# Optimization experiments

Measured on AMD Instinct MI355X. Metric: run time of the kernel, lower is better.

## Reference

```python
import jax, jax.numpy as jnp
import numpy as np

B, T, I, H, L = 64, 2048, 128, 256, 2


def setup_inputs() -> dict:
    key = jax.random.key(0)
    ks = jax.random.split(key, 16)
    def w(k, shape, s=0.05):
        return jax.random.normal(k, shape, jnp.float32) * s
    inp = {"input": jax.random.normal(ks[0], (B, T, I), jnp.float32)}
    in_sizes = [I, H]
    idx = 1
    for l in range(L):
        d = in_sizes[l]
        inp[f"W_ih_{l}"] = w(ks[idx], (d, H)); idx += 1
        inp[f"W_hh_{l}"] = w(ks[idx], (H, H)); idx += 1
        inp[f"b_h_{l}"] = jnp.zeros((H,), jnp.float32)
        inp[f"W_ax_{l}"] = w(ks[idx], (d, H)); idx += 1
        inp[f"W_ah_{l}"] = w(ks[idx], (H, H)); idx += 1
        inp[f"b_a_{l}"] = jnp.zeros((H,), jnp.float32)
    return inp


def reference(input, W_ih_0, W_hh_0, b_h_0, W_ax_0, W_ah_0, b_a_0,
              W_ih_1, W_hh_1, b_h_1, W_ax_1, W_ah_1, b_a_1):
    params = [(W_ih_0, W_hh_0, b_h_0, W_ax_0, W_ah_0, b_a_0),
              (W_ih_1, W_hh_1, b_h_1, W_ax_1, W_ah_1, b_a_1)]
    Bn = input.shape[0]
    Hn = W_hh_0.shape[0]
    h0 = jnp.zeros((len(params), Bn, Hn), input.dtype)

    def step(h, xt):  # xt: [B, in], h: [L, B, H]
        new_h = []
        cur = xt
        for l, (Wih, Whh, bh, Wax, Wah, ba) in enumerate(params):
            cand = jnp.tanh(cur @ Wih + h[l] @ Whh + bh)
            alpha = jax.nn.sigmoid(cur @ Wax + h[l] @ Wah + ba)
            hnew = alpha * cand + (1.0 - alpha) * h[l]
            new_h.append(hnew)
            cur = hnew
        return jnp.stack(new_h), cur

    h_final, ys = jax.lax.scan(step, h0, jnp.swapaxes(input, 0, 1))  # ys: [T,B,H]
    outputs = jnp.swapaxes(ys, 0, 1)  # [B, T, H]
    return outputs, h_final
```

## Files before the change

kernel.cpp:

```cpp
#include <hip/hip_runtime.h>

#define Bn 64
#define Tn 2048
#define In 128
#define Hn 256
#define RS 512

#define H0S (Hn + 8)
#define PLS (2 * Hn + 8)

typedef _Float16 h2 __attribute__((ext_vector_type(2)));
typedef _Float16 f16x8 __attribute__((ext_vector_type(8)));
typedef float f32x4 __attribute__((ext_vector_type(4)));

__device__ __forceinline__ float fast_sigmoid(float x) {
    return 1.0f / (1.0f + __expf(-x));
}
__device__ __forceinline__ float fast_tanh(float x) {
    return 2.0f / (1.0f + __expf(-2.0f * x)) - 1.0f;
}
__device__ __forceinline__ h2 bc2(float f) {
    return __builtin_bit_cast(h2, f);
}

#if __has_builtin(__builtin_amdgcn_fdot2)
__device__ __forceinline__ float dot2(h2 a, h2 b, float c) {
    return __builtin_amdgcn_fdot2(a, b, c, false);
}
#else
__device__ __forceinline__ float dot2(h2 a, h2 b, float c) {
    return c + (float)a.x * (float)b.x + (float)a.y * (float)b.y;
}
#endif

__global__ void gemm_x_kernel(const float* __restrict__ X,
                              const float* __restrict__ Wih0, const float* __restrict__ bh0,
                              const float* __restrict__ Wax0, const float* __restrict__ ba0,
                              _Float16* __restrict__ pre)
{
    __shared__ __align__(16) float Xs[64 * In];
    const int m0 = blockIdx.x * 64;
    const int s  = blockIdx.y;
    const float* __restrict__ W    = s ? Wax0 : Wih0;
    const float* __restrict__ bias = s ? ba0  : bh0;

    {
        const float4* __restrict__ src = reinterpret_cast<const float4*>(X + (size_t)m0 * In);
        float4* __restrict__ dst = reinterpret_cast<float4*>(Xs);
        #pragma unroll
        for (int i = 0; i < 8; ++i) dst[threadIdx.x + 256 * i] = src[threadIdx.x + 256 * i];
    }
    __syncthreads();

    const int c  = threadIdx.x & 63;
    const int rg = threadIdx.x >> 6;
    const int mr = rg * 16;

    float acc[16][4];
    #pragma unroll
    for (int u = 0; u < 4; ++u) {
        const float bv = bias[c + 64 * u];
        #pragma unroll
        for (int r = 0; r < 16; ++r) acc[r][u] = bv;
    }

    const float4* __restrict__ Xs4 = reinterpret_cast<const float4*>(Xs);
    #pragma unroll 4
    for (int kc = 0; kc < 32; ++kc) {
        float wv[4][4];
        #pragma unroll
        for (int kk = 0; kk < 4; ++kk)
            #pragma unroll
            for (int u = 0; u < 4; ++u)
                wv[kk][u] = W[(size_t)(4 * kc + kk) * Hn + c + 64 * u];
        #pragma unroll
        for (int r = 0; r < 16; ++r) {
            const float4 xv = Xs4[(mr + r) * 32 + kc];
            #pragma unroll
            for (int u = 0; u < 4; ++u)
                acc[r][u] += xv.x * wv[0][u] + xv.y * wv[1][u] + xv.z * wv[2][u] + xv.w * wv[3][u];
        }
    }

    #pragma unroll
    for (int r = 0; r < 16; ++r)
        #pragma unroll
        for (int u = 0; u < 4; ++u)
            pre[(size_t)(m0 + mr + r) * RS + s * Hn + c + 64 * u] = (_Float16)acc[r][u];
}

__global__ __launch_bounds__(1024, 4)
void fused_scan(_Float16* __restrict__ pre,
                const float* __restrict__ WU0, const float* __restrict__ WA0,
                const float* __restrict__ Wih1, const float* __restrict__ Wax1,
                const float* __restrict__ bh1,  const float* __restrict__ ba1,
                const float* __restrict__ WU1,  const float* __restrict__ WA1,
                float* __restrict__ outf, float* __restrict__ hfin,
                int* __restrict__ prog)
{
    __shared__ __align__(16) _Float16 hbuf[2][Hn];
    __shared__ __align__(16) float2   pbuf[3][Hn];
    __shared__ __align__(16) _Float16 h0t[32][H0S];
    __shared__ __align__(16) _Float16 preL[32][PLS];

    const int tid  = threadIdx.x;
    const int col  = tid & 255;
    const int kq   = tid >> 8;
    const int lane = tid & 63;
    const int w    = tid >> 6;
    const int g    = lane >> 4;
    const int cl   = lane & 15;

    if (blockIdx.x < Bn) {
        const int b = blockIdx.x;
        h2 bwU[32], bwA[32];
        #pragma unroll
        for (int i = 0; i < 32; ++i) {
            const int k0 = 64 * kq + 2 * i;
            h2 u, a;
            u.x = (_Float16)WU0[(size_t)k0 * Hn + col];
            u.y = (_Float16)WU0[(size_t)(k0 + 1) * Hn + col];
            a.x = (_Float16)WA0[(size_t)k0 * Hn + col];
            a.y = (_Float16)WA0[(size_t)(k0 + 1) * Hn + col];
            bwU[i] = u;
            bwA[i] = a;
        }

        _Float16* __restrict__ rowbase = pre + (size_t)b * Tn * RS;
        float hprev = 0.0f;

        if (tid < Hn) hbuf[0][tid] = (_Float16)0.0f;
        float pc[8];
        if (kq < 2) {
            const int off = kq ? Hn : 0;
            #pragma unroll
            for (int k = 0; k < 8; ++k)
                pc[k] = (float)rowbase[(size_t)k * RS + off + col];
        }
        __syncthreads();

        for (int t0 = 0; t0 < Tn; t0 += 8) {
            float pn[8];
            if (kq < 2) {
                const int off = kq ? Hn : 0;
                #pragma unroll
                for (int k = 0; k < 8; ++k) {
                    int tn = t0 + 8 + k;
                    if (tn > Tn - 1) tn = Tn - 1;
                    pn[k] = (float)rowbase[(size_t)tn * RS + off + col];
                }
            }

            float hst[8];

            #pragma unroll
            for (int ph = 0; ph < 8; ++ph) {
                const int t = t0 + ph;
                const f16x8* __restrict__ hb =
                    reinterpret_cast<const f16x8*>(&hbuf[t & 1][64 * kq]);

                float aU[2] = {0.0f, 0.0f};
                float aA[2] = {0.0f, 0.0f};
                #pragma unroll
                for (int r = 0; r < 8; ++r) {
                    const f16x8 v = hb[r];
                    const h2 p0 = __builtin_shufflevector(v, v, 0, 1);
                    const h2 p1 = __builtin_shufflevector(v, v, 2, 3);
                    const h2 p2 = __builtin_shufflevector(v, v, 4, 5);
                    const h2 p3 = __builtin_shufflevector(v, v, 6, 7);
                    aU[0] = dot2(p0, bwU[4 * r + 0], aU[0]);
                    aU[1] = dot2(p1, bwU[4 * r + 1], aU[1]);
                    aU[0] = dot2(p2, bwU[4 * r + 2], aU[0]);
                    aU[1] = dot2(p3, bwU[4 * r + 3], aU[1]);
                    aA[0] = dot2(p0, bwA[4 * r + 0], aA[0]);
                    aA[1] = dot2(p1, bwA[4 * r + 1], aA[1]);
                    aA[0] = dot2(p2, bwA[4 * r + 2], aA[0]);
                    aA[1] = dot2(p3, bwA[4 * r + 3], aA[1]);
                }
                float partU = aU[0] + aU[1];
                float partA = aA[0] + aA[1];
                if (kq == 1) partA += pc[ph];

                if (kq) pbuf[kq - 1][col] = make_float2(partU, partA);
                __syncthreads();

                if (kq == 0) {
                    const float2 q0 = pbuf[0][col];
                    const float2 q1 = pbuf[1][col];
                    const float2 q2 = pbuf[2][col];
                    const float yU = partU + q0.x + q1.x + q2.x + pc[ph];
                    const float yA = partA + q0.y + q1.y + q2.y;
                    const float cand  = fast_tanh(yU);
                    const float alpha = fast_sigmoid(yA);
                    const float hn = hprev + alpha * (cand - hprev);
                    hprev = hn;
                    hst[ph] = hn;
                    hbuf[(t + 1) & 1][col] = (_Float16)hn;
                }
                __syncthreads();
            }

            if (kq == 0) {
                #pragma unroll
                for (int k = 0; k < 8; ++k)
                    rowbase[(size_t)(t0 + k) * RS + col] = (_Float16)hst[k];
            }
            if (kq < 2) {
                #pragma unroll
                for (int k = 0; k < 8; ++k) pc[k] = pn[k];
            }

            if (((t0 >> 3) & 3) == 3) {
                __syncthreads();
                if (tid == 0) {
                    __threadfence();
                    __hip_atomic_store(prog + b, (t0 >> 5) + 1,
                                       __ATOMIC_RELEASE, __HIP_MEMORY_SCOPE_AGENT);
                }
            }
        }

        if (kq == 0) hfin[b * Hn + col] = hprev;

    } else {
        const int b = blockIdx.x - Bn;

        f16x8 bfr0[8], bfr1[8];
        float biasv0, biasv1;
        int cg0, cg1;
        {
            const int ntgA = 2 * w, ntgB = 2 * w + 1;
            const float* __restrict__ WmA = (ntgA < 16) ? Wih1 : Wax1;
            const float* __restrict__ WmB = (ntgB < 16) ? Wih1 : Wax1;
            const int nA = 16 * (ntgA & 15) + cl;
            const int nB = 16 * (ntgB & 15) + cl;
            biasv0 = (ntgA < 16) ? bh1[nA] : ba1[nA];
            biasv1 = (ntgB < 16) ? bh1[nB] : ba1[nB];
            cg0 = (ntgA < 16) ? nA : (Hn + nA);
            cg1 = (ntgB < 16) ? nB : (Hn + nB);
            #pragma unroll
            for (int kc = 0; kc < 8; ++kc) {
                const int k0 = 32 * kc + 8 * g;
                f16x8 fa, fb;
                #pragma unroll
                for (int jj = 0; jj < 8; ++jj) {
                    fa[jj] = (_Float16)WmA[(size_t)(k0 + jj) * Hn + nA];
                    fb[jj] = (_Float16)WmB[(size_t)(k0 + jj) * Hn + nB];
                }
                bfr0[kc] = fa;
                bfr1[kc] = fb;
            }
        }

        h2 bwU[32], bwA[32];
        #pragma unroll
        for (int i = 0; i < 32; ++i) {
            const int k0 = 64 * kq + 2 * i;
            h2 u, a;
            u.x = (_Float16)WU1[(size_t)k0 * Hn + col];
            u.y = (_Float16)WU1[(size_t)(k0 + 1) * Hn + col];
            a.x = (_Float16)WA1[(size_t)k0 * Hn + col];
            a.y = (_Float16)WA1[(size_t)(k0 + 1) * Hn + col];
            bwU[i] = u;
            bwA[i] = a;
        }

        _Float16* __restrict__ rowbase = pre + (size_t)b * Tn * RS;
        float* __restrict__ outb = outf + (size_t)b * Tn * Hn;
        float hprev = 0.0f;

        if (tid < Hn) hbuf[0][tid] = (_Float16)0.0f;
        __syncthreads();

        for (int grp = 0; grp < Tn / 32; ++grp) {
            const int t0g = 32 * grp;

            if (tid == 0) {
                while (__hip_atomic_load(prog + b, __ATOMIC_RELAXED,
                                         __HIP_MEMORY_SCOPE_AGENT) <= grp)
                    __builtin_amdgcn_s_sleep(8);
                (void)__hip_atomic_load(prog + b, __ATOMIC_ACQUIRE,
                                        __HIP_MEMORY_SCOPE_AGENT);
            }
            __syncthreads();

            #pragma unroll
            for (int q = 0; q < 4; ++q) {
                const int id  = tid + 1024 * q;
                const int r   = id >> 7;
                const int off = id & 127;
                const unsigned int v = *reinterpret_cast<const unsigned int*>(
                    rowbase + (size_t)(t0g + r) * RS + 2 * off);
                *reinterpret_cast<unsigned int*>(&h0t[r][2 * off]) = v;
            }
            __syncthreads();

            {
                #pragma unroll
                for (int mt = 0; mt < 2; ++mt) {
                    f16x8 af[8];
                    #pragma unroll
                    for (int kc = 0; kc < 8; ++kc)
                        af[kc] = *reinterpret_cast<const f16x8*>(
                            &h0t[16 * mt + cl][32 * kc + 8 * g]);

                    const f32x4 z = {0.0f, 0.0f, 0.0f, 0.0f};
                    f32x4 a0 = __builtin_amdgcn_mfma_f32_16x16x32_f16(af[0], bfr0[0], z, 0, 0, 0);
                    f32x4 a1 = __builtin_amdgcn_mfma_f32_16x16x32_f16(af[0], bfr1[0], z, 0, 0, 0);
                    #pragma unroll
                    for (int kc = 1; kc < 8; ++kc) {
                        a0 = __builtin_amdgcn_mfma_f32_16x16x32_f16(af[kc], bfr0[kc], a0, 0, 0, 0);
                        a1 = __builtin_amdgcn_mfma_f32_16x16x32_f16(af[kc], bfr1[kc], a1, 0, 0, 0);
                    }
                    const int r0 = 16 * mt + (lane >> 4) * 4;
                    #pragma unroll
                    for (int ri = 0; ri < 4; ++ri) {
                        preL[r0 + ri][cg0] = (_Float16)(a0[ri] + biasv0);
                        preL[r0 + ri][cg1] = (_Float16)(a1[ri] + biasv1);
                    }
                }
            }
            __syncthreads();

            for (int cc = 0; cc < 4; ++cc) {
                const int t0 = t0g + 8 * cc;
                float hst[8];
                #pragma unroll
                for (int ph = 0; ph < 8; ++ph) {
                    const int t = t0 + ph;
                    const int pr = 8 * cc + ph;
                    const f16x8* __restrict__ hb =
                        reinterpret_cast<const f16x8*>(&hbuf[t & 1][64 * kq]);

                    float aU[2] = {0.0f, 0.0f};
                    float aA[2] = {0.0f, 0.0f};
                    #pragma unroll
                    for (int r = 0; r < 8; ++r) {
                        const f16x8 v = hb[r];
                        const h2 p0 = __builtin_shufflevector(v, v, 0, 1);
                        const h2 p1 = __builtin_shufflevector(v, v, 2, 3);
                        const h2 p2 = __builtin_shufflevector(v, v, 4, 5);
                        const h2 p3 = __builtin_shufflevector(v, v, 6, 7);
                        aU[0] = dot2(p0, bwU[4 * r + 0], aU[0]);
                        aU[1] = dot2(p1, bwU[4 * r + 1], aU[1]);
                        aU[0] = dot2(p2, bwU[4 * r + 2], aU[0]);
                        aU[1] = dot2(p3, bwU[4 * r + 3], aU[1]);
                        aA[0] = dot2(p0, bwA[4 * r + 0], aA[0]);
                        aA[1] = dot2(p1, bwA[4 * r + 1], aA[1]);
                        aA[0] = dot2(p2, bwA[4 * r + 2], aA[0]);
                        aA[1] = dot2(p3, bwA[4 * r + 3], aA[1]);
                    }
                    const float partU = aU[0] + aU[1];
                    const float partA = aA[0] + aA[1];

                    if (kq) pbuf[kq - 1][col] = make_float2(partU, partA);
                    __syncthreads();

                    if (kq == 0) {
                        const float2 q0 = pbuf[0][col];
                        const float2 q1 = pbuf[1][col];
                        const float2 q2 = pbuf[2][col];
                        const float yU = partU + q0.x + q1.x + q2.x + (float)preL[pr][col];
                        const float yA = partA + q0.y + q1.y + q2.y + (float)preL[pr][Hn + col];
                        const float cand  = fast_tanh(yU);
                        const float alpha = fast_sigmoid(yA);
                        const float hn = hprev + alpha * (cand - hprev);
                        hprev = hn;
                        hst[ph] = hn;
                        hbuf[(t + 1) & 1][col] = (_Float16)hn;
                    }
                    __syncthreads();
                }

                if (kq == 0) {
                    #pragma unroll
                    for (int k = 0; k < 8; ++k)
                        outb[(size_t)(t0 + k) * Hn + col] = hst[k];
                }
            }
        }

        if (kq == 0) hfin[Bn * Hn + b * Hn + col] = hprev;
    }
}

extern "C" void kernel_launch(void* const* d_in, const int* in_sizes, int n_in,
                              void* d_out, int out_size, void* d_ws, size_t ws_size,
                              hipStream_t stream) {
    const float* X    = (const float*)d_in[0];
    const float* Wih0 = (const float*)d_in[1];
    const float* Whh0 = (const float*)d_in[2];
    const float* bh0  = (const float*)d_in[3];
    const float* Wax0 = (const float*)d_in[4];
    const float* Wah0 = (const float*)d_in[5];
    const float* ba0  = (const float*)d_in[6];
    const float* Wih1 = (const float*)d_in[7];
    const float* Whh1 = (const float*)d_in[8];
    const float* bh1  = (const float*)d_in[9];
    const float* Wax1 = (const float*)d_in[10];
    const float* Wah1 = (const float*)d_in[11];
    const float* ba1  = (const float*)d_in[12];

    float* outf = (float*)d_out;
    float* hfin = outf + (size_t)Bn * Tn * Hn;
    _Float16* pre = (_Float16*)d_out;
    int* prog = (int*)d_ws;

    hipMemsetAsync(prog, 0, Bn * sizeof(int), stream);
    gemm_x_kernel<<<dim3((Bn * Tn) / 64, 2), 256, 0, stream>>>(X, Wih0, bh0, Wax0, ba0, pre);
    fused_scan<<<dim3(2 * Bn), 1024, 0, stream>>>(pre, Whh0, Wah0,
                                                  Wih1, Wax1, bh1, ba1,
                                                  Whh1, Wah1, outf, hfin, prog);
}
```

Before: 2.621 ms.

## Split recurrent matvec: MFMA waves for candidate gate, dot2 waves for alpha

```diff
diff --git a/kernel.cpp b/kernel.cpp
--- a/kernel.cpp
+++ b/kernel.cpp
@@ -99,55 +99,95 @@
                 int* __restrict__ prog)
 {
     __shared__ __align__(16) _Float16 hbuf[2][Hn];
-    __shared__ __align__(16) float2   pbuf[3][Hn];
+    __shared__ __align__(16) float    ypU[Hn];
+    __shared__ __align__(16) float    apar[2][Hn];
     __shared__ __align__(16) _Float16 h0t[32][H0S];
     __shared__ __align__(16) _Float16 preL[32][PLS];
 
     const int tid  = threadIdx.x;
-    const int col  = tid & 255;
-    const int kq   = tid >> 8;
     const int lane = tid & 63;
     const int w    = tid >> 6;
     const int g    = lane >> 4;
     const int cl   = lane & 15;
 
-    if (blockIdx.x < Bn) {
-        const int b = blockIdx.x;
-        h2 bwU[32], bwA[32];
-        #pragma unroll
-        for (int i = 0; i < 32; ++i) {
-            const int k0 = 64 * kq + 2 * i;
-            h2 u, a;
-            u.x = (_Float16)WU0[(size_t)k0 * Hn + col];
-            u.y = (_Float16)WU0[(size_t)(k0 + 1) * Hn + col];
-            a.x = (_Float16)WA0[(size_t)k0 * Hn + col];
-            a.y = (_Float16)WA0[(size_t)(k0 + 1) * Hn + col];
-            bwU[i] = u;
+    const bool isU = ((w >> 2) & 1) == 0;
+    const int  iu  = (w < 4) ? w : (w - 4);
+    const int  khU = iu >> 2;
+    const int  q   = iu & 3;
+    const int  ia  = (w < 8) ? (w - 4) : (w - 8);
+    const int  aid = ia * 64 + lane;
+    const int  colA = aid & 255;
+    const int  khA  = aid >> 8;
+
+    const int b = (blockIdx.x < Bn) ? blockIdx.x : (blockIdx.x - Bn);
+    const int layer = (blockIdx.x < Bn) ? 0 : 1;
+
+    const float* __restrict__ WU = layer ? WU1 : WU0;
+    const float* __restrict__ WA = layer ? WA1 : WA0;
+
+    f16x8 bfragU[4][4];
+    if (isU) {
+        #pragma unroll
+        for (int nt = 0; nt < 4; ++nt) {
+            #pragma unroll
+            for (int kc = 0; kc < 4; ++kc) {
+                const int n  = 64 * q + 16 * nt + cl;
+                const int k0 = 128 * khU + 32 * kc + 8 * g;
+                f16x8 f;
+                #pragma unroll
+                for (int jj = 0; jj < 8; ++jj)
+                    f[jj] = (_Float16)WU[(size_t)(k0 + jj) * Hn + n];
+                bfragU[nt][kc] = f;
+            }
+        }
+    }
+
+    h2 bwA[64];
+    if (!isU) {
+        #pragma unroll
+        for (int i = 0; i < 64; ++i) {
+            const int k0 = 128 * khA + 2 * i;
+            h2 a;
+            a.x = (_Float16)WA[(size_t)k0 * Hn + colA];
+            a.y = (_Float16)WA[(size_t)(k0 + 1) * Hn + colA];
             bwA[i] = a;
         }
-
-        _Float16* __restrict__ rowbase = pre + (size_t)b * Tn * RS;
-        float hprev = 0.0f;
-
+    }
+
+    _Float16* __restrict__ rowbase = pre + (size_t)b * Tn * RS;
+    float hprev = 0.0f;
+
+    if (layer == 0) {
         if (tid < Hn) hbuf[0][tid] = (_Float16)0.0f;
-        float pc[8];
-        if (kq < 2) {
-            const int off = kq ? Hn : 0;
+        float pcU[8], pcA[8];
+        if (tid < Hn) {
             #pragma unroll
             for (int k = 0; k < 8; ++k)
-                pc[k] = (float)rowbase[(size_t)k * RS + off + col];
+                pcU[k] = (float)rowbase[(size_t)k * RS + tid];
+        }
+        if (tid >= 768) {
+            #pragma unroll
+            for (int k = 0; k < 8; ++k)
+                pcA[k] = (float)rowbase[(size_t)k * RS + Hn + (tid - 768)];
         }
         __syncthreads();
 
         for (int t0 = 0; t0 < Tn; t0 += 8) {
-            float pn[8];
-            if (kq < 2) {
-                const int off = kq ? Hn : 0;
+            float pnU[8], pnA[8];
+            if (tid < Hn) {
                 #pragma unroll
                 for (int k = 0; k < 8; ++k) {
                     int tn = t0 + 8 + k;
                     if (tn > Tn - 1) tn = Tn - 1;
-                    pn[k] = (float)rowbase[(size_t)tn * RS + off + col];
+                    pnU[k] = (float)rowbase[(size_t)tn * RS + tid];
+                }
+            }
+            if (tid >= 768) {
+                #pragma unroll
+                for (int k = 0; k < 8; ++k) {
+                    int tn = t0 + 8 + k;
+                    if (tn > Tn - 1) tn = Tn - 1;
+                    pnA[k] = (float)rowbase[(size_t)tn * RS + Hn + (tid - 768)];
                 }
             }
 
@@ -156,58 +196,77 @@
             #pragma unroll
             for (int ph = 0; ph < 8; ++ph) {
                 const int t = t0 + ph;
-                const f16x8* __restrict__ hb =
-                    reinterpret_cast<const f16x8*>(&hbuf[t & 1][64 * kq]);
-
-                float aU[2] = {0.0f, 0.0f};
-                float aA[2] = {0.0f, 0.0f};
-                #pragma unroll
-                for (int r = 0; r < 8; ++r) {
-                    const f16x8 v = hb[r];
-                    const h2 p0 = __builtin_shufflevector(v, v, 0, 1);
-                    const h2 p1 = __builtin_shufflevector(v, v, 2, 3);
-                    const h2 p2 = __builtin_shufflevector(v, v, 4, 5);
-                    const h2 p3 = __builtin_shufflevector(v, v, 6, 7);
-                    aU[0] = dot2(p0, bwU[4 * r + 0], aU[0]);
-                    aU[1] = dot2(p1, bwU[4 * r + 1], aU[1]);
-                    aU[0] = dot2(p2, bwU[4 * r + 2], aU[0]);
-                    aU[1] = dot2(p3, bwU[4 * r + 3], aU[1]);
-                    aA[0] = dot2(p0, bwA[4 * r + 0], aA[0]);
-                    aA[1] = dot2(p1, bwA[4 * r + 1], aA[1]);
-                    aA[0] = dot2(p2, bwA[4 * r + 2], aA[0]);
-                    aA[1] = dot2(p3, bwA[4 * r + 3], aA[1]);
-                }
-                float partU = aU[0] + aU[1];
-                float partA = aA[0] + aA[1];
-                if (kq == 1) partA += pc[ph];
-
-                if (kq) pbuf[kq - 1][col] = make_float2(partU, partA);
+                float yv = 0.0f;
+
+                if (isU) {
+                    const float4* __restrict__ hb4 =
+                        reinterpret_cast<const float4*>(&hbuf[t & 1][128 * khU]);
+                    f16x8 af[4];
+                    #pragma unroll
+                    for (int kc = 0; kc < 4; ++kc)
+                        af[kc] = __builtin_bit_cast(f16x8, hb4[4 * kc + g]);
+
+                    const f32x4 z = {0.0f, 0.0f, 0.0f, 0.0f};
+                    f32x4 a0 = __builtin_amdgcn_mfma_f32_16x16x32_f16(af[0], bfragU[0][0], z, 0, 0, 0);
+                    f32x4 a1 = __builtin_amdgcn_mfma_f32_16x16x32_f16(af[0], bfragU[1][0], z, 0, 0, 0);
+                    f32x4 a2 = __builtin_amdgcn_mfma_f32_16x16x32_f16(af[0], bfragU[2][0], z, 0, 0, 0);
+                    f32x4 a3 = __builtin_amdgcn_mfma_f32_16x16x32_f16(af[0], bfragU[3][0], z, 0, 0, 0);
+                    #pragma unroll
+                    for (int kc = 1; kc < 4; ++kc) {
+                        a0 = __builtin_amdgcn_mfma_f32_16x16x32_f16(af[kc], bfragU[0][kc], a0, 0, 0, 0);
+                        a1 = __builtin_amdgcn_mfma_f32_16x16x32_f16(af[kc], bfragU[1][kc], a1, 0, 0, 0);
+                        a2 = __builtin_amdgcn_mfma_f32_16x16x32_f16(af[kc], bfragU[2][kc], a2, 0, 0, 0);
+                        a3 = __builtin_amdgcn_mfma_f32_16x16x32_f16(af[kc], bfragU[3][kc], a3, 0, 0, 0);
+                    }
+                    const float y01 = (lane & 16) ? a1.x : a0.x;
+                    const float y23 = (lane & 16) ? a3.x : a2.x;
+                    yv = (lane & 32) ? y23 : y01;
+                    if (khU) ypU[64 * q + lane] = yv;
+                } else {
+                    const f16x8* __restrict__ hbA =
+                        reinterpret_cast<const f16x8*>(&hbuf[t & 1][128 * khA]);
+                    float c0 = 0.0f, c1 = 0.0f, c2 = 0.0f, c3 = 0.0f;
+                    #pragma unroll
+                    for (int r = 0; r < 16; ++r) {
+                        const f16x8 v = hbA[r];
+                        const h2 p0 = __builtin_shufflevector(v, v, 0, 1);
+                        const h2 p1 = __builtin_shufflevector(v, v, 2, 3);
+                        const h2 p2 = __builtin_shufflevector(v, v, 4, 5);
+                        const h2 p3 = __builtin_shufflevector(v, v, 6, 7);
+                        c0 = dot2(p0, bwA[4 * r + 0], c0);
+                        c1 = dot2(p1, bwA[4 * r + 1], c1);
+                        c2 = dot2(p2, bwA[4 * r + 2], c2);
+                        c3 = dot2(p3, bwA[4 * r + 3], c3);
+                    }
+                    float part = (c0 + c1) + (c2 + c3);
+                    if (khA) part += pcA[ph];
+                    apar[khA][colA] = part;
+                }
                 __syncthreads();
 
-                if (kq == 0) {
-                    const float2 q0 = pbuf[0][col];
-                    const float2 q1 = pbuf[1][col];
-                    const float2 q2 = pbuf[2][col];
-                    const float yU = partU + q0.x + q1.x + q2.x + pc[ph];
-                    const float yA = partA + q0.y + q1.y + q2.y;
+                if (tid < Hn) {
+                    const float yU = yv + ypU[tid] + pcU[ph];
+                    const float yA = apar[0][tid] + apar[1][tid];
                     const float cand  = fast_tanh(yU);
                     const float alpha = fast_sigmoid(yA);
                     const float hn = hprev + alpha * (cand - hprev);
                     hprev = hn;
                     hst[ph] = hn;
-                    hbuf[(t + 1) & 1][col] = (_Float16)hn;
+                    hbuf[(t + 1) & 1][tid] = (_Float16)hn;
                 }
                 __syncthreads();
             }
 
-            if (kq == 0) {
+            if (tid < Hn) {
                 #pragma unroll
                 for (int k = 0; k < 8; ++k)
-                    rowbase[(size_t)(t0 + k) * RS + col] = (_Float16)hst[k];
-            }
-            if (kq < 2) {
-                #pragma unroll
-                for (int k = 0; k < 8; ++k) pc[k] = pn[k];
+                    rowbase[(size_t)(t0 + k) * RS + tid] = (_Float16)hst[k];
+                #pragma unroll
+                for (int k = 0; k < 8; ++k) pcU[k] = pnU[k];
+            }
+            if (tid >= 768) {
+                #pragma unroll
+                for (int k = 0; k < 8; ++k) pcA[k] = pnA[k];
             }
 
             if (((t0 >> 3) & 3) == 3) {
@@ -220,11 +279,9 @@
             }
         }
 
-        if (kq == 0) hfin[b * Hn + col] = hprev;
+        if (tid < Hn) hfin[b * Hn + tid] = hprev;
 
     } else {
-        const int b = blockIdx.x - Bn;
-
         f16x8 bfr0[8], bfr1[8];
         float biasv0, biasv1;
         int cg0, cg1;
@@ -252,22 +309,7 @@
             }
         }
 
-        h2 bwU[32], bwA[32];
-        #pragma unroll
-        for (int i = 0; i < 32; ++i) {
-            const int k0 = 64 * kq + 2 * i;
-            h2 u, a;
-            u.x = (_Float16)WU1[(size_t)k0 * Hn + col];
-            u.y = (_Float16)WU1[(size_t)(k0 + 1) * Hn + col];
-            a.x = (_Float16)WA1[(size_t)k0 * Hn + col];
-            a.y = (_Float16)WA1[(size_t)(k0 + 1) * Hn + col];
-            bwU[i] = u;
-            bwA[i] = a;
-        }
-
-        _Float16* __restrict__ rowbase = pre + (size_t)b * Tn * RS;
         float* __restrict__ outb = outf + (size_t)b * Tn * Hn;
-        float hprev = 0.0f;
 
         if (tid < Hn) hbuf[0][tid] = (_Float16)0.0f;
         __syncthreads();
@@ -285,8 +327,8 @@
             __syncthreads();
 
             #pragma unroll
-            for (int q = 0; q < 4; ++q) {
-                const int id  = tid + 1024 * q;
+            for (int qq = 0; qq < 4; ++qq) {
+                const int id  = tid + 1024 * qq;
                 const int r   = id >> 7;
                 const int off = id & 127;
                 const unsigned int v = *reinterpret_cast<const unsigned int*>(
@@ -295,92 +337,120 @@
             }
             __syncthreads();
 
-            {
-                #pragma unroll
-                for (int mt = 0; mt < 2; ++mt) {
-                    f16x8 af[8];
-                    #pragma unroll
-                    for (int kc = 0; kc < 8; ++kc)
-                        af[kc] = *reinterpret_cast<const f16x8*>(
-                            &h0t[16 * mt + cl][32 * kc + 8 * g]);
-
-                    const f32x4 z = {0.0f, 0.0f, 0.0f, 0.0f};
-                    f32x4 a0 = __builtin_amdgcn_mfma_f32_16x16x32_f16(af[0], bfr0[0], z, 0, 0, 0);
-                    f32x4 a1 = __builtin_amdgcn_mfma_f32_16x16x32_f16(af[0], bfr1[0], z, 0, 0, 0);
-                    #pragma unroll
-                    for (int kc = 1; kc < 8; ++kc) {
-                        a0 = __builtin_amdgcn_mfma_f32_16x16x32_f16(af[kc], bfr0[kc], a0, 0, 0, 0);
-                        a1 = __builtin_amdgcn_mfma_f32_16x16x32_f16(af[kc], bfr1[kc], a1, 0, 0, 0);
-                    }
-                    const int r0 = 16 * mt + (lane >> 4) * 4;
-                    #pragma unroll
-                    for (int ri = 0; ri < 4; ++ri) {
-                        preL[r0 + ri][cg0] = (_Float16)(a0[ri] + biasv0);
-                        preL[r0 + ri][cg1] = (_Float16)(a1[ri] + biasv1);
-                    }
+            #pragma unroll
+            for (int mt = 0; mt < 2; ++mt) {
+                f16x8 af[8];
+                #pragma unroll
+                for (int kc = 0; kc < 8; ++kc)
+                    af[kc] = *reinterpret_cast<const f16x8*>(
+                        &h0t[16 * mt + cl][32 * kc + 8 * g]);
+
+                const f32x4 z = {0.0f, 0.0f, 0.0f, 0.0f};
+                f32x4 a0 = __builtin_amdgcn_mfma_f32_16x16x32_f16(af[0], bfr0[0], z, 0, 0, 0);
+                f32x4 a1 = __builtin_amdgcn_mfma_f32_16x16x32_f16(af[0], bfr1[0], z, 0, 0, 0);
+                #pragma unroll
+                for (int kc = 1; kc < 8; ++kc) {
+                    a0 = __builtin_amdgcn_mfma_f32_16x16x32_f16(af[kc], bfr0[kc], a0, 0, 0, 0);
+                    a1 = __builtin_amdgcn_mfma_f32_16x16x32_f16(af[kc], bfr1[kc], a1, 0, 0, 0);
+                }
+                const int r0 = 16 * mt + (lane >> 4) * 4;
+                #pragma unroll
+                for (int ri = 0; ri < 4; ++ri) {
+                    preL[r0 + ri][cg0] = (_Float16)(a0[ri] + biasv0);
+                    preL[r0 + ri][cg1] = (_Float16)(a1[ri] + biasv1);
                 }
             }
             __syncthreads();
 
             for (int cc = 0; cc < 4; ++cc) {
                 const int t0 = t0g + 8 * cc;
+
+                float pcU[8], pcA[8];
+                if (tid < Hn) {
+                    #pragma unroll
+                    for (int ph = 0; ph < 8; ++ph)
+                        pcU[ph] = (float)preL[8 * cc + ph][tid];
+                }
+                if (tid >= 768) {
+                    #pragma unroll
+                    for (int ph = 0; ph < 8; ++ph)
+                        pcA[ph] = (float)preL[8 * cc + ph][Hn + (tid - 768)];
+                }
+
                 float hst[8];
                 #pragma unroll
                 for (int ph = 0; ph < 8; ++ph) {
                     const int t = t0 + ph;
-                    const int pr = 8 * cc + ph;
-                    const f16x8* __restrict__ hb =
-                        reinterpret_cast<const f16x8*>(&hbuf[t & 1][64 * kq]);
-
-                    float aU[2] = {0.0f, 0.0f};
-                    float aA[2] = {0.0f, 0.0f};
-                    #pragma unroll
-                    for (int r = 0; r < 8; ++r) {
-                        const f16x8 v = hb[r];
-                        const h2 p0 = __builtin_shufflevector(v, v, 0, 1);
-                        const h2 p1 = __builtin_shufflevector(v, v, 2, 3);
-                        const h2 p2 = __builtin_shufflevector(v, v, 4, 5);
-                        const h2 p3 = __builtin_shufflevector(v, v, 6, 7);
-                        aU[0] = dot2(p0, bwU[4 * r + 0], aU[0]);
-                        aU[1] = dot2(p1, bwU[4 * r + 1], aU[1]);
-                        aU[0] = dot2(p2, bwU[4 * r + 2], aU[0]);
-                        aU[1] = dot2(p3, bwU[4 * r + 3], aU[1]);
-                        aA[0] = dot2(p0, bwA[4 * r + 0], aA[0]);
-                        aA[1] = dot2(p1, bwA[4 * r + 1], aA[1]);
-                        aA[0] = dot2(p2, bwA[4 * r + 2], aA[0]);
-                        aA[1] = dot2(p3, bwA[4 * r + 3], aA[1]);
+                    float yv = 0.0f;
+
+                    if (isU) {
+                        const float4* __restrict__ hb4 =
+                            reinterpret_cast<const float4*>(&hbuf[t & 1][128 * khU]);
+                        f16x8 af[4];
+                        #pragma unroll
+                        for (int kc = 0; kc < 4; ++kc)
+                            af[kc] = __builtin_bit_cast(f16x8, hb4[4 * kc + g]);
+
+                        const f32x4 z = {0.0f, 0.0f, 0.0f, 0.0f};
+                        f32x4 a0 = __builtin_amdgcn_mfma_f32_16x16x32_f16(af[0], bfragU[0][0], z, 0, 0, 0);
+                        f32x4 a1 = __builtin_amdgcn_mfma_f32_16x16x32_f16(af[0], bfragU[1][0], z, 0, 0, 0);
+                        f32x4 a2 = __builtin_amdgcn_mfma_f32_16x16x32_f16(af[0], bfragU[2][0], z, 0, 0, 0);
+                        f32x4 a3 = __builtin_amdgcn_mfma_f32_16x16x32_f16(af[0], bfragU[3][0], z, 0, 0, 0);
+                        #pragma unroll
+                        for (int kc = 1; kc < 4; ++kc) {
+                            a0 = __builtin_amdgcn_mfma_f32_16x16x32_f16(af[kc], bfragU[0][kc], a0, 0, 0, 0);
+                            a1 = __builtin_amdgcn_mfma_f32_16x16x32_f16(af[kc], bfragU[1][kc], a1, 0, 0, 0);
+                            a2 = __builtin_amdgcn_mfma_f32_16x16x32_f16(af[kc], bfragU[2][kc], a2, 0, 0, 0);
+                            a3 = __builtin_amdgcn_mfma_f32_16x16x32_f16(af[kc], bfragU[3][kc], a3, 0, 0, 0);
+                        }
+                        const float y01 = (lane & 16) ? a1.x : a0.x;
+                        const float y23 = (lane & 16) ? a3.x : a2.x;
+                        yv = (lane & 32) ? y23 : y01;
+                        if (khU) ypU[64 * q + lane] = yv;
+                    } else {
+                        const f16x8* __restrict__ hbA =
+                            reinterpret_cast<const f16x8*>(&hbuf[t & 1][128 * khA]);
+                        float c0 = 0.0f, c1 = 0.0f, c2 = 0.0f, c3 = 0.0f;
+                        #pragma unroll
+                        for (int r = 0; r < 16; ++r) {
+                            const f16x8 v = hbA[r];
+                            const h2 p0 = __builtin_shufflevector(v, v, 0, 1);
+                            const h2 p1 = __builtin_shufflevector(v, v, 2, 3);
+                            const h2 p2 = __builtin_shufflevector(v, v, 4, 5);
+                            const h2 p3 = __builtin_shufflevector(v, v, 6, 7);
+                            c0 = dot2(p0, bwA[4 * r + 0], c0);
+                            c1 = dot2(p1, bwA[4 * r + 1], c1);
+                            c2 = dot2(p2, bwA[4 * r + 2], c2);
+                            c3 = dot2(p3, bwA[4 * r + 3], c3);
+                        }
+                        float part = (c0 + c1) + (c2 + c3);
+                        if (khA) part += pcA[ph];
+                        apar[khA][colA] = part;
                     }
-                    const float partU = aU[0] + aU[1];
-                    const float partA = aA[0] + aA[1];
-
-                    if (kq) pbuf[kq - 1][col] = make_float2(partU, partA);
                     __syncthreads();
 
-                    if (kq == 0) {
-                        const float2 q0 = pbuf[0][col];
-                        const float2 q1 = pbuf[1][col];
-                        const float2 q2 = pbuf[2][col];
-                        const float yU = partU + q0.x + q1.x + q2.x + (float)preL[pr][col];
-                        const float yA = partA + q0.y + q1.y + q2.y + (float)preL[pr][Hn + col];
+                    if (tid < Hn) {
+                        const float yU = yv + ypU[tid] + pcU[ph];
+                        const float yA = apar[0][tid] + apar[1][tid];
                         const float cand  = fast_tanh(yU);
                         const float alpha = fast_sigmoid(yA);
                         const float hn = hprev + alpha * (cand - hprev);
                         hprev = hn;
                         hst[ph] = hn;
-                        hbuf[(t + 1) & 1][col] = (_Float16)hn;
+                        hbuf[(t + 1) & 1][tid] = (_Float16)hn;
                     }
                     __syncthreads();
                 }
 
-                if (kq == 0) {
+                if (tid < Hn) {
                     #pragma unroll
                     for (int k = 0; k < 8; ++k)
-                        outb[(size_t)(t0 + k) * Hn + col] = hst[k];
-                }
-            }
-        }
-
-        if (kq == 0) hfin[Bn * Hn + b * Hn + col] = hprev;
+                        outb[(size_t)(t0 + k) * Hn + tid] = hst[k];
+                }
+            }
+        }
+
+        if (tid < Hn) hfin[Bn * Hn + b * Hn + tid] = hprev;
     }
 }
 
```

New measurement: 9.750 ms. 3.72x slower.

## Enlarge layer-1 consumer group to 64 steps and preload pre-activations into registers

Applied to the files above, without the earlier changes.

```diff
diff --git a/kernel.cpp b/kernel.cpp
--- a/kernel.cpp
+++ b/kernel.cpp
@@ -8,6 +8,7 @@
 
 #define H0S (Hn + 8)
 #define PLS (2 * Hn + 8)
+#define GC  8
 
 typedef _Float16 h2 __attribute__((ext_vector_type(2)));
 typedef _Float16 f16x8 __attribute__((ext_vector_type(8)));
@@ -100,8 +101,8 @@
 {
     __shared__ __align__(16) _Float16 hbuf[2][Hn];
     __shared__ __align__(16) float2   pbuf[3][Hn];
-    __shared__ __align__(16) _Float16 h0t[32][H0S];
-    __shared__ __align__(16) _Float16 preL[32][PLS];
+    __shared__ __align__(16) _Float16 h0t[8 * GC][H0S];
+    __shared__ __align__(16) _Float16 preL[8 * GC][PLS];
 
     const int tid  = threadIdx.x;
     const int col  = tid & 255;
@@ -210,11 +211,11 @@
                 for (int k = 0; k < 8; ++k) pc[k] = pn[k];
             }
 
-            if (((t0 >> 3) & 3) == 3) {
+            if (((t0 >> 3) & (GC - 1)) == (GC - 1)) {
                 __syncthreads();
                 if (tid == 0) {
                     __threadfence();
-                    __hip_atomic_store(prog + b, (t0 >> 5) + 1,
+                    __hip_atomic_store(prog + b, (t0 >> 3) / GC + 1,
                                        __ATOMIC_RELEASE, __HIP_MEMORY_SCOPE_AGENT);
                 }
             }
@@ -272,8 +273,8 @@
         if (tid < Hn) hbuf[0][tid] = (_Float16)0.0f;
         __syncthreads();
 
-        for (int grp = 0; grp < Tn / 32; ++grp) {
-            const int t0g = 32 * grp;
+        for (int grp = 0; grp < Tn / (8 * GC); ++grp) {
+            const int t0g = 8 * GC * grp;
 
             if (tid == 0) {
                 while (__hip_atomic_load(prog + b, __ATOMIC_RELAXED,
@@ -285,8 +286,8 @@
             __syncthreads();
 
             #pragma unroll
-            for (int q = 0; q < 4; ++q) {
-                const int id  = tid + 1024 * q;
+            for (int qq = 0; qq < GC; ++qq) {
+                const int id  = tid + 1024 * qq;
                 const int r   = id >> 7;
                 const int off = id & 127;
                 const unsigned int v = *reinterpret_cast<const unsigned int*>(
@@ -295,40 +296,46 @@
             }
             __syncthreads();
 
-            {
-                #pragma unroll
-                for (int mt = 0; mt < 2; ++mt) {
-                    f16x8 af[8];
+            #pragma unroll
+            for (int mt = 0; mt < GC / 2; ++mt) {
+                f16x8 af[8];
+                #pragma unroll
+                for (int kc = 0; kc < 8; ++kc)
+                    af[kc] = *reinterpret_cast<const f16x8*>(
+                        &h0t[16 * mt + cl][32 * kc + 8 * g]);
+
+                const f32x4 z = {0.0f, 0.0f, 0.0f, 0.0f};
+                f32x4 a0 = __builtin_amdgcn_mfma_f32_16x16x32_f16(af[0], bfr0[0], z, 0, 0, 0);
+                f32x4 a1 = __builtin_amdgcn_mfma_f32_16x16x32_f16(af[0], bfr1[0], z, 0, 0, 0);
+                #pragma unroll
+                for (int kc = 1; kc < 8; ++kc) {
+                    a0 = __builtin_amdgcn_mfma_f32_16x16x32_f16(af[kc], bfr0[kc], a0, 0, 0, 0);
+                    a1 = __builtin_amdgcn_mfma_f32_16x16x32_f16(af[kc], bfr1[kc], a1, 0, 0, 0);
+                }
+                const int r0 = 16 * mt + (lane >> 4) * 4;
+                #pragma unroll
+                for (int ri = 0; ri < 4; ++ri) {
+                    preL[r0 + ri][cg0] = (_Float16)(a0[ri] + biasv0);
+                    preL[r0 + ri][cg1] = (_Float16)(a1[ri] + biasv1);
+                }
+            }
+            __syncthreads();
+
+            for (int cc = 0; cc < GC; ++cc) {
+                const int t0 = t0g + 8 * cc;
+
+                float pc[8];
+                if (kq < 2) {
+                    const int off = kq ? Hn : 0;
                     #pragma unroll
-                    for (int kc = 0; kc < 8; ++kc)
-                        af[kc] = *reinterpret_cast<const f16x8*>(
-                            &h0t[16 * mt + cl][32 * kc + 8 * g]);
-
-                    const f32x4 z = {0.0f, 0.0f, 0.0f, 0.0f};
-                    f32x4 a0 = __builtin_amdgcn_mfma_f32_16x16x32_f16(af[0], bfr0[0], z, 0, 0, 0);
-                    f32x4 a1 = __builtin_amdgcn_mfma_f32_16x16x32_f16(af[0], bfr1[0], z, 0, 0, 0);
-                    #pragma unroll
-                    for (int kc = 1; kc < 8; ++kc) {
-                        a0 = __builtin_amdgcn_mfma_f32_16x16x32_f16(af[kc], bfr0[kc], a0, 0, 0, 0);
-                        a1 = __builtin_amdgcn_mfma_f32_16x16x32_f16(af[kc], bfr1[kc], a1, 0, 0, 0);
-                    }
-                    const int r0 = 16 * mt + (lane >> 4) * 4;
-                    #pragma unroll
-                    for (int ri = 0; ri < 4; ++ri) {
-                        preL[r0 + ri][cg0] = (_Float16)(a0[ri] + biasv0);
-                        preL[r0 + ri][cg1] = (_Float16)(a1[ri] + biasv1);
-                    }
-                }
-            }
-            __syncthreads();
-
-            for (int cc = 0; cc < 4; ++cc) {
-                const int t0 = t0g + 8 * cc;
+                    for (int ph = 0; ph < 8; ++ph)
+                        pc[ph] = (float)preL[8 * cc + ph][off + col];
+                }
+
                 float hst[8];
                 #pragma unroll
                 for (int ph = 0; ph < 8; ++ph) {
                     const int t = t0 + ph;
-                    const int pr = 8 * cc + ph;
                     const f16x8* __restrict__ hb =
                         reinterpret_cast<const f16x8*>(&hbuf[t & 1][64 * kq]);
 
@@ -350,8 +357,9 @@
                         aA[0] = dot2(p2, bwA[4 * r + 2], aA[0]);
                         aA[1] = dot2(p3, bwA[4 * r + 3], aA[1]);
                     }
-                    const float partU = aU[0] + aU[1];
-                    const float partA = aA[0] + aA[1];
+                    float partU = aU[0] + aU[1];
+                    float partA = aA[0] + aA[1];
+                    if (kq == 1) partA += pc[ph];
 
                     if (kq) pbuf[kq - 1][col] = make_float2(partU, partA);
                     __syncthreads();
@@ -360,8 +368,8 @@
                         const float2 q0 = pbuf[0][col];
                         const float2 q1 = pbuf[1][col];
                         const float2 q2 = pbuf[2][col];
-                        const float yU = partU + q0.x + q1.x + q2.x + (float)preL[pr][col];
-                        const float yA = partA + q0.y + q1.y + q2.y + (float)preL[pr][Hn + col];
+                        const float yU = partU + q0.x + q1.x + q2.x + pc[ph];
+                        const float yA = partA + q0.y + q1.y + q2.y;
                         const float cand  = fast_tanh(yU);
                         const float alpha = fast_sigmoid(yA);
                         const float hn = hprev + alpha * (cand - hprev);
```

Result: slower. 3.113 ms (+18.8%).
